# Optimization experiments

Hardware: AMD Instinct MI355X
Metric: run time of the kernel (lower is better)

The kernel has to match this reference:

```python
import jax, jax.numpy as jnp
import numpy as np


def _gru_dirs(x, h, w_ih, w_hh, b_ih, b_hh):
    # One GRU step for both directions at once (seq_len==1 per original loop).
    # x: [N, in], h: [2, N, H]; w_ih: [2, 3H, in], w_hh: [2, 3H, H], biases [2, 3H]
    gi = jnp.einsum('ni,dgi->dng', x, w_ih) + b_ih[:, None, :]
    gh = jnp.einsum('dnh,dgh->dng', h, w_hh) + b_hh[:, None, :]
    H = h.shape[-1]
    ir, iz, inn = gi[..., :H], gi[..., H:2 * H], gi[..., 2 * H:]
    hr, hz, hn = gh[..., :H], gh[..., H:2 * H], gh[..., 2 * H:]
    r = jax.nn.sigmoid(ir + hr)
    z = jax.nn.sigmoid(iz + hz)
    n = jnp.tanh(inn + r * hn)
    return (1.0 - z) * n + z * h


def setup_inputs() -> dict:
    key = jax.random.key(0)
    ks = jax.random.split(key, 6)
    V, E, H, NL = 32000, 1024, 512, 2  # vocab, input_size, hidden_size, num_layers
    N, L = 32, 512
    s = 0.05
    x = jax.random.randint(ks[0], (N, L), 0, V)
    emb = jax.random.normal(ks[1], (V, E), dtype=jnp.float32) * s
    w_ih = jax.random.normal(ks[2], (NL, 2, 3 * H, E), dtype=jnp.float32) * s
    w_hh = jax.random.normal(ks[3], (NL, 2, 3 * H, H), dtype=jnp.float32) * s
    b_ih = jax.random.normal(ks[4], (NL, 2, 3 * H), dtype=jnp.float32) * s
    b_hh = jax.random.normal(ks[5], (NL, 2, 3 * H), dtype=jnp.float32) * s
    return {"x": x, "emb": emb, "w_ih": w_ih, "w_hh": w_hh, "b_ih": b_ih, "b_hh": b_hh}


def reference(x, emb, w_ih, w_hh, b_ih, b_hh):
    # Because the torch code calls the bidirectional GRU one timestep at a time
    # with a carried hidden, BOTH directions scan left-to-right over the sequence.
    N, L = x.shape
    num_layers = w_ih.shape[0]
    H = w_hh.shape[-1]
    h0 = jnp.zeros((num_layers, 2, N, H), dtype=emb.dtype)

    def step(h, xt):
        layer_in = emb[xt]  # [N, E] embedding lookup for this timestep
        new_h = []
        for l in range(num_layers):  # fixed small layer loop
            hl = _gru_dirs(layer_in, h[l], w_ih[l], w_hh[l], b_ih[l], b_hh[l])
            new_h.append(hl)
            layer_in = jnp.concatenate([hl[0], hl[1]], axis=-1)  # [N, 2H]
        hs = jnp.stack(new_h)  # [num_layers, 2, N, H]
        return hs, (layer_in, hs)

    _, (outs, hiddens) = jax.lax.scan(step, h0, x.T)  # scan over L timesteps
    outputs = jnp.transpose(outs, (1, 0, 2))  # [N, L, 2H]
    hiddens = hiddens.reshape(L, num_layers * 2, N, H)  # [L, 2*num_layers, N, H]
    return outputs, hiddens
```

## Files before the change

### kernel.cpp

```cpp
#include <hip/hip_runtime.h>
#include <hip/hip_bf16.h>

using u16 = unsigned short;
using u32 = unsigned int;
using bf16x8 = __attribute__((ext_vector_type(8))) __bf16;
using f32x4  = __attribute__((ext_vector_type(4))) float;
using u32x4  = __attribute__((ext_vector_type(4))) u32;

#define GLP(p) ((const __attribute__((address_space(1))) void*)(p))
#define LDSP(p) ((__attribute__((address_space(3))) void*)(p))

__device__ __forceinline__ float bf2f(u16 u) {
    union { float f; u32 i; } v; v.i = ((u32)u) << 16; return v.f;
}
__device__ __forceinline__ u16 f2bf(float f) {
    union { float f; u32 i; } v; v.f = f;
    u32 r = v.i + 0x7FFFu + ((v.i >> 16) & 1u);
    return (u16)(r >> 16);
}

__device__ __forceinline__ u32 ld_sc01_u32(const u32* p) {
    u32 v;
    asm volatile("global_load_dword %0, %1, off sc0 sc1\n\ts_waitcnt vmcnt(0)"
                 : "=v"(v) : "v"(p) : "memory");
    return v;
}
__device__ __forceinline__ void st_sc01_u32(u32* p, u32 v) {
    asm volatile("global_store_dword %0, %1, off sc0 sc1" :: "v"(p), "v"(v) : "memory");
}
__device__ __forceinline__ void st_sc01_u16(u16* p, u16 v) {
    asm volatile("global_store_short %0, %1, off sc0 sc1" :: "v"(p), "v"(v) : "memory");
}
__device__ __forceinline__ void st_sc01_u32x4(u16* p, u32x4 v) {
    asm volatile("global_store_dwordx4 %0, %1, off sc0 sc1" :: "v"(p), "v"(v) : "memory");
}

__global__ void k_gather(const int* __restrict__ x, const float* __restrict__ emb,
                         u16* __restrict__ X0) {
    int gid = blockIdx.x * blockDim.x + threadIdx.x;
    if (gid >= 16384 * 256) return;
    int e4 = gid << 2;
    int m = e4 >> 10, k = e4 & 1023;
    int t = m >> 5, n = m & 31;
    int tok = x[n * 512 + t];
    float4 v = *reinterpret_cast<const float4*>(emb + ((size_t)tok << 10) + k);
    ushort4 o;
    o.x = f2bf(v.x); o.y = f2bf(v.y); o.z = f2bf(v.z); o.w = f2bf(v.w);
    *reinterpret_cast<ushort4*>(X0 + (size_t)e4) = o;
}

__global__ void k_f32bf16(const float* __restrict__ s, u16* __restrict__ d, int n4) {
    int gid = blockIdx.x * blockDim.x + threadIdx.x;
    if (gid >= n4) return;
    float4 v = reinterpret_cast<const float4*>(s)[gid];
    ushort4 o;
    o.x = f2bf(v.x); o.y = f2bf(v.y); o.z = f2bf(v.z); o.w = f2bf(v.w);
    reinterpret_cast<ushort4*>(d)[gid] = o;
}

template<int LAYER>
__device__ __forceinline__ void gru_body(char* smem, int d, int wg,
    const u16* __restrict__ Gi, const u16* __restrict__ Whh_l,
    const float* __restrict__ bhh_l, u16* __restrict__ hbuf,
    u16* __restrict__ X1, float* __restrict__ hid, float* __restrict__ outp,
    u32* __restrict__ flags, u32* __restrict__ xflags, const u32* __restrict__ gdone)
{
    char* hS          = smem;
    float (*ghs)[196] = (float(*)[196])(smem + 32768);
    u16 (*gis)[208]   = (u16(*)[208])(smem + 57856);
    float* bhh_s      = (float*)(smem + 71168);
    u16* hvS          = (u16*)(smem + 71936);
    const int tid = threadIdx.x;
    const int lane = tid & 63, w = tid >> 6;
    const int j0 = wg * 64;
    const int g = w >> 2;
    const int lr = lane & 15, lk = lane >> 4;

    if (tid < 192) {
        int g2 = tid >> 6, jj = tid & 63;
        bhh_s[tid] = bhh_l[d * 1536 + g2 * 512 + j0 + jj];
    }
    bf16x8 wf[16];
    {
        const int joff = (w & 3) * 16;
        const u16* wr = Whh_l + (size_t)(d * 1536 + g * 512 + j0 + joff + lr) * 512 + lk * 8;
        #pragma unroll
        for (int kt = 0; kt < 16; ++kt)
            wf[kt] = *reinterpret_cast<const bf16x8*>(wr + kt * 32);
    }
    __syncthreads();

    u32* myflag = flags + (d * 8 + wg) * 32;
    const u32* wflag = flags + (d * 8 + (w & 7)) * 32;
    u32* myxflag = (LAYER == 0) ? xflags + (d * 8 + wg) * 32 : nullptr;

    const int c8 = (lane & 7) * 8;
    const int rb = lane >> 3;
    const int colu = w * 64 + c8;
    const int ci0 = (tid - 512) * 3;

    float hp0 = 0.f, hp1 = 0.f, hp2 = 0.f;
    u32 g_seen = 0;

    for (int t = 0; t < 512; ++t) {
        if (w < 8) {
            if (t > 0) {
                long long tt0 = __builtin_amdgcn_s_memrealtime();
                while (ld_sc01_u32(wflag) < (u32)t) {
                    __builtin_amdgcn_s_sleep(1);
                    if (__builtin_amdgcn_s_memrealtime() - tt0 > 2000) {
                        if (lane == 0)
                            __hip_atomic_store(myflag, (u32)t, __ATOMIC_RELEASE,
                                               __HIP_MEMORY_SCOPE_AGENT);
                        tt0 = __builtin_amdgcn_s_memrealtime();
                    }
                }
            }
            const u16* hb = hbuf + ((size_t)d * 2 + ((t + 1) & 1)) * 16384;
            u32x4 v0, v1, v2, v3;
            asm volatile("global_load_dwordx4 %0, %1, off sc0 sc1"
                         : "=v"(v0) : "v"(hb + (size_t)(rb)      * 512 + colu));
            asm volatile("global_load_dwordx4 %0, %1, off sc0 sc1"
                         : "=v"(v1) : "v"(hb + (size_t)(rb + 8)  * 512 + colu));
            asm volatile("global_load_dwordx4 %0, %1, off sc0 sc1"
                         : "=v"(v2) : "v"(hb + (size_t)(rb + 16) * 512 + colu));
            asm volatile("global_load_dwordx4 %0, %1, off sc0 sc1"
                         : "=v"(v3) : "v"(hb + (size_t)(rb + 24) * 512 + colu));
            asm volatile("s_waitcnt vmcnt(0)" ::: "memory");
            const int cb = colu * 2;
            *reinterpret_cast<u32x4*>(hS + (rb)      * 1024 + (cb ^ (((rb)      & 15) << 4))) = v0;
            *reinterpret_cast<u32x4*>(hS + (rb + 8)  * 1024 + (cb ^ (((rb + 8)  & 15) << 4))) = v1;
            *reinterpret_cast<u32x4*>(hS + (rb + 16) * 1024 + (cb ^ (((rb + 16) & 15) << 4))) = v2;
            *reinterpret_cast<u32x4*>(hS + (rb + 24) * 1024 + (cb ^ (((rb + 24) & 15) << 4))) = v3;
        } else {
            u32 yneed = (u32)(t >> 2);
            if (g_seen <= yneed) {
                const u32* gp = gdone + yneed;
                long long T0 = __builtin_amdgcn_s_memrealtime();
                while (ld_sc01_u32(gp) == 0) {
                    __builtin_amdgcn_s_sleep(1);
                    if (__builtin_amdgcn_s_memrealtime() - T0 > 2000000) break;
                }
                g_seen = yneed + 1;
            }
            u32x4 gq[3];
            int nbs[3], gcs[3];
            #pragma unroll
            for (int i = 0; i < 3; ++i) {
                int ci = ci0 + i;
                nbs[i] = ci / 24; gcs[i] = ci % 24;
                const u16* gp = Gi + (size_t)(t * 32 + nbs[i]) * 3072 + d * 1536
                              + (gcs[i] >> 3) * 512 + j0 + (gcs[i] & 7) * 8;
                asm volatile("global_load_dwordx4 %0, %1, off sc0 sc1"
                             : "=v"(gq[i]) : "v"(gp));
            }
            asm volatile("s_waitcnt vmcnt(0)" ::: "memory");
            #pragma unroll
            for (int i = 0; i < 3; ++i)
                *reinterpret_cast<u32x4*>(&gis[nbs[i]][gcs[i] * 8]) = gq[i];
        }
        __syncthreads();

        f32x4 acc0 = {0.f, 0.f, 0.f, 0.f}, acc1 = acc0;
        #pragma unroll
        for (int kt = 0; kt < 16; ++kt) {
            int boff = (lk * 16 + kt * 64) ^ (lr << 4);
            bf16x8 a0 = *reinterpret_cast<const bf16x8*>(hS + lr * 1024 + boff);
            bf16x8 a1 = *reinterpret_cast<const bf16x8*>(hS + (16 + lr) * 1024 + boff);
            acc0 = __builtin_amdgcn_mfma_f32_16x16x32_bf16(a0, wf[kt], acc0, 0, 0, 0);
            acc1 = __builtin_amdgcn_mfma_f32_16x16x32_bf16(a1, wf[kt], acc1, 0, 0, 0);
        }
        int colg = w * 16 + lr;
        float bv = bhh_s[colg];
        #pragma unroll
        for (int q = 0; q < 4; ++q) {
            ghs[lk * 4 + q][colg]      = acc0[q] + bv;
            ghs[16 + lk * 4 + q][colg] = acc1[q] + bv;
        }
        __syncthreads();

        u16* hbw = hbuf + ((size_t)d * 2 + (t & 1)) * 16384;
        #pragma unroll
        for (int rep = 0; rep < 3; ++rep) {
            int e = tid + rep * 768;
            if (e < 2048) {
                int j = e & 63, nb = e >> 6;
                float gr = bf2f(gis[nb][j])       + ghs[nb][j];
                float gz = bf2f(gis[nb][64 + j])  + ghs[nb][64 + j];
                float r = 1.f / (1.f + __expf(-gr));
                float z = 1.f / (1.f + __expf(-gz));
                float ng = tanhf(bf2f(gis[nb][128 + j]) + r * ghs[nb][128 + j]);
                float hp = (rep == 0) ? hp0 : (rep == 1) ? hp1 : hp2;
                float hv = (1.f - z) * ng + z * hp;
                if (rep == 0) hp0 = hv; else if (rep == 1) hp1 = hv; else hp2 = hv;
                u16 hb16 = f2bf(hv);
                st_sc01_u16(hbw + (size_t)nb * 512 + j0 + j, hb16);
                hvS[nb * 64 + j] = hb16;
            }
        }
        asm volatile("s_waitcnt vmcnt(0)" ::: "memory");
        __syncthreads();
        if (tid == 16)
            st_sc01_u32(myflag, (u32)(t + 1));

        if (tid >= 512) {
            int q = tid - 512, nb = q >> 3, j8 = (q & 7) * 8;
            union { u32x4 v; u16 s[8]; } h8;
            h8.v = *reinterpret_cast<const u32x4*>(hvS + nb * 64 + j8);
            float f0 = bf2f(h8.s[0]), f1 = bf2f(h8.s[1]), f2 = bf2f(h8.s[2]), f3 = bf2f(h8.s[3]);
            float f4 = bf2f(h8.s[4]), f5 = bf2f(h8.s[5]), f6 = bf2f(h8.s[6]), f7 = bf2f(h8.s[7]);
            float* hp = hid + ((size_t)(t * 4 + LAYER * 2 + d) * 32 + nb) * 512 + j0 + j8;
            *reinterpret_cast<float4*>(hp)     = make_float4(f0, f1, f2, f3);
            *reinterpret_cast<float4*>(hp + 4) = make_float4(f4, f5, f6, f7);
            if (LAYER == 0) {
                u16* xp = X1 + (size_t)(t * 32 + nb) * 1024 + (size_t)d * 512 + j0 + j8;
                st_sc01_u32x4(xp, h8.v);
            } else {
                float* op = outp + ((size_t)nb * 512 + t) * 1024 + (size_t)d * 512 + j0 + j8;
                *reinterpret_cast<float4*>(op)     = make_float4(f0, f1, f2, f3);
                *reinterpret_cast<float4*>(op + 4) = make_float4(f4, f5, f6, f7);
            }
        }
        if (LAYER == 0 && (t & 3) == 3) {
            asm volatile("s_waitcnt vmcnt(0)" ::: "memory");
            __syncthreads();
            if (tid == 17)
                st_sc01_u32(myxflag, (u32)(t + 1));
        }
    }
}

__device__ __forceinline__ void chaser_body(char* smem, int cw,
    const u16* __restrict__ A, const u16* __restrict__ B,
    const float* __restrict__ bias, u16* __restrict__ Gi,
    const u32* __restrict__ xflags, u32* __restrict__ cnt, u32* __restrict__ done)
{
    u16* As = (u16*)smem;
    u16* Bs = (u16*)(smem + 16384);
    const int tid = threadIdx.x;
    const int lane = tid & 63, wid = tid >> 6;
    const int wm = wid & 1, wn = wid >> 1;
    const int lr = lane & 15, lk = lane >> 4;

    for (int T = cw; T < 4096; T += 48) {
        const int y = T >> 5, x = T & 31;
        if (xflags && tid < 16) {
            const u32* fp = xflags + tid * 32;
            u32 target = 4u * (u32)y + 4u;
            long long T0 = __builtin_amdgcn_s_memrealtime();
            while (ld_sc01_u32(fp) < target) {
                __builtin_amdgcn_s_sleep(4);
                if (__builtin_amdgcn_s_memrealtime() - T0 > 2000000) break;
            }
        }
        __syncthreads();

        f32x4 zero = {0.f, 0.f, 0.f, 0.f};
        f32x4 acc[4][2];
        #pragma unroll
        for (int i = 0; i < 4; ++i) { acc[i][0] = zero; acc[i][1] = zero; }

        for (int k0 = 0; k0 < 1024; k0 += 64) {
            #pragma unroll
            for (int r = 0; r < 5; ++r) {
                int c = wid * 5 + r;
                if (c < 16) {
                    int o = c * 1024 + lane * 16;
                    int row = o >> 7, kb = o & 127;
                    int kbs = kb ^ ((row & 7) << 4);
                    const char* s = (const char*)A + ((size_t)(y * 128 + row) * 1024 + k0) * 2 + kbs;
                    __builtin_amdgcn_global_load_lds(GLP(s), LDSP((char*)As + c * 1024), 16, 0, 0);
                } else if (c < 28) {
                    int c2 = c - 16;
                    int o = c2 * 1024 + lane * 16;
                    int row = o >> 7, kb = o & 127;
                    int kbs = kb ^ ((row & 7) << 4);
                    const char* s = (const char*)B + ((size_t)(x * 96 + row) * 1024 + k0) * 2 + kbs;
                    __builtin_amdgcn_global_load_lds(GLP(s), LDSP((char*)Bs + c2 * 1024), 16, 0, 0);
                }
            }
            __syncthreads();
            if (wid < 6) {
                #pragma unroll
                for (int kk = 0; kk < 2; ++kk) {
                    bf16x8 af[4], bfr[2];
                    int kb = kk * 64 + lk * 16;
                    #pragma unroll
                    for (int i = 0; i < 4; ++i) {
                        int rowA = wm * 64 + i * 16 + lr;
                        af[i] = *reinterpret_cast<const bf16x8*>((const char*)As + rowA * 128 + (kb ^ ((rowA & 7) << 4)));
                    }
                    #pragma unroll
                    for (int j = 0; j < 2; ++j) {
                        int rowB = wn * 32 + j * 16 + lr;
                        bfr[j] = *reinterpret_cast<const bf16x8*>((const char*)Bs + rowB * 128 + (kb ^ ((rowB & 7) << 4)));
                    }
                    #pragma unroll
                    for (int i = 0; i < 4; ++i)
                        #pragma unroll
                        for (int j = 0; j < 2; ++j)
                            acc[i][j] = __builtin_amdgcn_mfma_f32_16x16x32_bf16(af[i], bfr[j], acc[i][j], 0, 0, 0);
                }
            }
            __syncthreads();
        }
        if (wid < 6) {
            #pragma unroll
            for (int j = 0; j < 2; ++j) {
                int col = x * 96 + wn * 32 + j * 16 + lr;
                float bv = bias[col];
                #pragma unroll
                for (int i = 0; i < 4; ++i) {
                    int rowb = y * 128 + wm * 64 + i * 16 + lk * 4;
                    #pragma unroll
                    for (int q = 0; q < 4; ++q)
                        st_sc01_u16(Gi + (size_t)(rowb + q) * 3072 + col, f2bf(acc[i][j][q] + bv));
                }
            }
        }
        asm volatile("s_waitcnt vmcnt(0)" ::: "memory");
        __syncthreads();
        if (tid == 0) {
            u32 old = __hip_atomic_fetch_add(&cnt[y], 1u, __ATOMIC_RELAXED,
                                             __HIP_MEMORY_SCOPE_AGENT);
            if (old == 31u)
                st_sc01_u32((u32*)&done[y], 1u);
        }
    }
}

__global__ __launch_bounds__(768, 2) void k_fused(
    u16* __restrict__ Gi,
    const u16* __restrict__ X0, const u16* __restrict__ Wih,
    const float* __restrict__ b_ih,
    const u16* __restrict__ Whh, const float* __restrict__ bhh,
    u16* __restrict__ hbuf0, u16* __restrict__ hbuf1,
    u16* __restrict__ X1,
    float* __restrict__ hid, float* __restrict__ outp,
    u32* __restrict__ flags0, u32* __restrict__ flags1,
    u32* __restrict__ xflags,
    u32* __restrict__ g0cnt, u32* __restrict__ g0done,
    u32* __restrict__ g1cnt, u32* __restrict__ g1done)
{
    __shared__ __align__(16) char smem[76032];
    int bid = blockIdx.x;
    if (bid < 16) {
        gru_body<0>(smem, bid >> 3, bid & 7, Gi, Whh, bhh, hbuf0,
                    X1, hid, outp, flags0, xflags, g0done);
    } else if (bid < 64) {
        chaser_body(smem, bid - 16, X0, Wih, b_ih, Gi, nullptr, g0cnt, g0done);
    } else if (bid < 112) {
        chaser_body(smem, bid - 64, X1, Wih + (size_t)3072 * 1024, b_ih + 3072,
                    Gi, xflags, g1cnt, g1done);
    } else {
        int b = bid - 112;
        gru_body<1>(smem, b >> 3, b & 7, Gi, Whh + (size_t)3072 * 512, bhh + 3072,
                    hbuf1, nullptr, hid, outp, flags1, nullptr, g1done);
    }
}

extern "C" void kernel_launch(void* const* d_in, const int* in_sizes, int n_in,
                              void* d_out, int out_size, void* d_ws, size_t ws_size,
                              hipStream_t stream) {
    const int*   x    = (const int*)d_in[0];
    const float* emb  = (const float*)d_in[1];
    const float* w_ih = (const float*)d_in[2];
    const float* w_hh = (const float*)d_in[3];
    const float* b_ih = (const float*)d_in[4];
    const float* b_hh = (const float*)d_in[5];
    float* outp = (float*)d_out;
    float* hid  = outp + (size_t)32 * 512 * 1024;

    char* ws = (char*)d_ws;
    u16* X0     = (u16*)(ws);
    u16* X1     = (u16*)(ws + 33554432);
    u16* Wih    = (u16*)(ws + 67108864);
    u16* Whh    = (u16*)(ws + 79691776);
    u16* Gi     = (u16*)(ws + 85983232);
    u16* hbuf0  = (u16*)(ws + 186646528);
    u16* hbuf1  = (u16*)(ws + 186777600);
    u32* flags0 = (u32*)(ws + 186908672);
    u32* flags1 = (u32*)(ws + 186910720);
    u32* xflags = (u32*)(ws + 186912768);
    u32* g0cnt  = (u32*)(ws + 186914816);
    u32* g0done = (u32*)(ws + 186915328);
    u32* g1cnt  = (u32*)(ws + 186915840);
    u32* g1done = (u32*)(ws + 186916352);

    k_gather<<<16384, 256, 0, stream>>>(x, emb, X0);
    k_f32bf16<<<(1572864 + 255) / 256, 256, 0, stream>>>(w_ih, Wih, 1572864);
    k_f32bf16<<<( 786432 + 255) / 256, 256, 0, stream>>>(w_hh, Whh, 786432);

    (void)hipMemsetAsync(hbuf0, 0, 270336, stream);

    k_fused<<<128, 768, 0, stream>>>(Gi, X0, Wih, b_ih, Whh, b_hh,
                                     hbuf0, hbuf1, X1, hid, outp,
                                     flags0, flags1, xflags,
                                     g0cnt, g0done, g1cnt, g1done);
}
```

Before: 2.141 ms.

## Replace per-step block barrier with per-wave LDS ready flags and fast gates

Each wave that loads a slice of h into LDS now posts its own ready flag. The MFMA loop spins on each flag before consuming that k-slice, so the full __syncthreads before the recurrent matmul is gone and compute can start while other slices are still arriving. The global flag spin drops s_sleep and checks the timer only every 16 polls. The gate math switches to rcp/exp-based sigmoid and tanh and handles two outputs per thread, storing them as packed u32. This targets latency on the serial recurrence, at the cost of busier LDS and global spinning and slightly less accurate activations.

```diff
diff --git a/kernel.cpp b/kernel.cpp
--- a/kernel.cpp
+++ b/kernel.cpp
@@ -33,6 +33,14 @@
 }
 __device__ __forceinline__ void st_sc01_u32x4(u16* p, u32x4 v) {
     asm volatile("global_store_dwordx4 %0, %1, off sc0 sc1" :: "v"(p), "v"(v) : "memory");
+}
+
+__device__ __forceinline__ float sigm(float x) {
+    return __builtin_amdgcn_rcpf(1.f + __expf(-x));
+}
+__device__ __forceinline__ float tanh_fast(float x) {
+    float e = __expf(-2.f * x);
+    return (1.f - e) * __builtin_amdgcn_rcpf(1.f + e);
 }
 
 __global__ void k_gather(const int* __restrict__ x, const float* __restrict__ emb,
@@ -70,6 +78,7 @@
     u16 (*gis)[208]   = (u16(*)[208])(smem + 57856);
     float* bhh_s      = (float*)(smem + 71168);
     u16* hvS          = (u16*)(smem + 71936);
+    volatile u32* rdy = (volatile u32*)(smem + 76032);
     const int tid = threadIdx.x;
     const int lane = tid & 63, w = tid >> 6;
     const int j0 = wg * 64;
@@ -80,6 +89,7 @@
         int g2 = tid >> 6, jj = tid & 63;
         bhh_s[tid] = bhh_l[d * 1536 + g2 * 512 + j0 + jj];
     }
+    if (tid < 8) rdy[tid] = 0;
     bf16x8 wf[16];
     {
         const int joff = (w & 3) * 16;
@@ -92,27 +102,29 @@
 
     u32* myflag = flags + (d * 8 + wg) * 32;
     const u32* wflag = flags + (d * 8 + (w & 7)) * 32;
-    u32* myxflag = (LAYER == 0) ? xflags + (d * 8 + wg) * 32 : nullptr;
 
     const int c8 = (lane & 7) * 8;
     const int rb = lane >> 3;
     const int colu = w * 64 + c8;
     const int ci0 = (tid - 512) * 3;
 
-    float hp0 = 0.f, hp1 = 0.f, hp2 = 0.f;
+    float hpv[4] = {0.f, 0.f, 0.f, 0.f};
     u32 g_seen = 0;
 
     for (int t = 0; t < 512; ++t) {
         if (w < 8) {
             if (t > 0) {
                 long long tt0 = __builtin_amdgcn_s_memrealtime();
+                int k = 0;
                 while (ld_sc01_u32(wflag) < (u32)t) {
-                    __builtin_amdgcn_s_sleep(1);
-                    if (__builtin_amdgcn_s_memrealtime() - tt0 > 2000) {
-                        if (lane == 0)
-                            __hip_atomic_store(myflag, (u32)t, __ATOMIC_RELEASE,
-                                               __HIP_MEMORY_SCOPE_AGENT);
-                        tt0 = __builtin_amdgcn_s_memrealtime();
+                    if (++k >= 16) {
+                        k = 0;
+                        if (__builtin_amdgcn_s_memrealtime() - tt0 > 2000) {
+                            if (lane == 0)
+                                __hip_atomic_store(myflag, (u32)t, __ATOMIC_RELEASE,
+                                                   __HIP_MEMORY_SCOPE_AGENT);
+                            tt0 = __builtin_amdgcn_s_memrealtime();
+                        }
                     }
                 }
             }
@@ -132,6 +144,9 @@
             *reinterpret_cast<u32x4*>(hS + (rb + 8)  * 1024 + (cb ^ (((rb + 8)  & 15) << 4))) = v1;
             *reinterpret_cast<u32x4*>(hS + (rb + 16) * 1024 + (cb ^ (((rb + 16) & 15) << 4))) = v2;
             *reinterpret_cast<u32x4*>(hS + (rb + 24) * 1024 + (cb ^ (((rb + 24) & 15) << 4))) = v3;
+            asm volatile("s_waitcnt lgkmcnt(0)" ::: "memory");
+            __builtin_amdgcn_sched_barrier(0);
+            if (lane == 0) rdy[w] = (u32)(t + 1);
         } else {
             u32 yneed = (u32)(t >> 2);
             if (g_seen <= yneed) {
@@ -159,16 +174,22 @@
             for (int i = 0; i < 3; ++i)
                 *reinterpret_cast<u32x4*>(&gis[nbs[i]][gcs[i] * 8]) = gq[i];
         }
-        __syncthreads();
 
         f32x4 acc0 = {0.f, 0.f, 0.f, 0.f}, acc1 = acc0;
         #pragma unroll
-        for (int kt = 0; kt < 16; ++kt) {
-            int boff = (lk * 16 + kt * 64) ^ (lr << 4);
-            bf16x8 a0 = *reinterpret_cast<const bf16x8*>(hS + lr * 1024 + boff);
-            bf16x8 a1 = *reinterpret_cast<const bf16x8*>(hS + (16 + lr) * 1024 + boff);
-            acc0 = __builtin_amdgcn_mfma_f32_16x16x32_bf16(a0, wf[kt], acc0, 0, 0, 0);
-            acc1 = __builtin_amdgcn_mfma_f32_16x16x32_bf16(a1, wf[kt], acc1, 0, 0, 0);
+        for (int s = 0; s < 8; ++s) {
+            while (rdy[s] < (u32)(t + 1)) {}
+            __builtin_amdgcn_sched_barrier(0);
+            int b0 = (lk * 16 + (2 * s) * 64) ^ (lr << 4);
+            int b1 = (lk * 16 + (2 * s + 1) * 64) ^ (lr << 4);
+            bf16x8 a00 = *reinterpret_cast<const bf16x8*>(hS + lr * 1024 + b0);
+            bf16x8 a10 = *reinterpret_cast<const bf16x8*>(hS + (16 + lr) * 1024 + b0);
+            bf16x8 a01 = *reinterpret_cast<const bf16x8*>(hS + lr * 1024 + b1);
+            bf16x8 a11 = *reinterpret_cast<const bf16x8*>(hS + (16 + lr) * 1024 + b1);
+            acc0 = __builtin_amdgcn_mfma_f32_16x16x32_bf16(a00, wf[2 * s],     acc0, 0, 0, 0);
+            acc1 = __builtin_amdgcn_mfma_f32_16x16x32_bf16(a10, wf[2 * s],     acc1, 0, 0, 0);
+            acc0 = __builtin_amdgcn_mfma_f32_16x16x32_bf16(a01, wf[2 * s + 1], acc0, 0, 0, 0);
+            acc1 = __builtin_amdgcn_mfma_f32_16x16x32_bf16(a11, wf[2 * s + 1], acc1, 0, 0, 0);
         }
         int colg = w * 16 + lr;
         float bv = bhh_s[colg];
@@ -181,21 +202,22 @@
 
         u16* hbw = hbuf + ((size_t)d * 2 + (t & 1)) * 16384;
         #pragma unroll
-        for (int rep = 0; rep < 3; ++rep) {
-            int e = tid + rep * 768;
-            if (e < 2048) {
-                int j = e & 63, nb = e >> 6;
-                float gr = bf2f(gis[nb][j])       + ghs[nb][j];
-                float gz = bf2f(gis[nb][64 + j])  + ghs[nb][64 + j];
-                float r = 1.f / (1.f + __expf(-gr));
-                float z = 1.f / (1.f + __expf(-gz));
-                float ng = tanhf(bf2f(gis[nb][128 + j]) + r * ghs[nb][128 + j]);
-                float hp = (rep == 0) ? hp0 : (rep == 1) ? hp1 : hp2;
-                float hv = (1.f - z) * ng + z * hp;
-                if (rep == 0) hp0 = hv; else if (rep == 1) hp1 = hv; else hp2 = hv;
-                u16 hb16 = f2bf(hv);
-                st_sc01_u16(hbw + (size_t)nb * 512 + j0 + j, hb16);
-                hvS[nb * 64 + j] = hb16;
+        for (int rep = 0; rep < 2; ++rep) {
+            int e2 = tid + rep * 768;
+            if (e2 < 1024) {
+                int jp = (e2 & 31) * 2, nb = e2 >> 5;
+                float r0 = sigm(bf2f(gis[nb][jp])      + ghs[nb][jp]);
+                float r1 = sigm(bf2f(gis[nb][jp + 1])  + ghs[nb][jp + 1]);
+                float z0 = sigm(bf2f(gis[nb][64 + jp])     + ghs[nb][64 + jp]);
+                float z1 = sigm(bf2f(gis[nb][64 + jp + 1]) + ghs[nb][64 + jp + 1]);
+                float n0 = tanh_fast(bf2f(gis[nb][128 + jp])     + r0 * ghs[nb][128 + jp]);
+                float n1 = tanh_fast(bf2f(gis[nb][128 + jp + 1]) + r1 * ghs[nb][128 + jp + 1]);
+                float hv0 = (1.f - z0) * n0 + z0 * hpv[rep * 2];
+                float hv1 = (1.f - z1) * n1 + z1 * hpv[rep * 2 + 1];
+                hpv[rep * 2] = hv0; hpv[rep * 2 + 1] = hv1;
+                u32 packed = (u32)f2bf(hv0) | ((u32)f2bf(hv1) << 16);
+                st_sc01_u32((u32*)(hbw + (size_t)nb * 512 + j0 + jp), packed);
+                *reinterpret_cast<u32*>(hvS + nb * 64 + jp) = packed;
             }
         }
         asm volatile("s_waitcnt vmcnt(0)" ::: "memory");
@@ -225,7 +247,7 @@
             asm volatile("s_waitcnt vmcnt(0)" ::: "memory");
             __syncthreads();
             if (tid == 17)
-                st_sc01_u32(myxflag, (u32)(t + 1));
+                st_sc01_u32(xflags + (d * 8 + wg) * 32, (u32)(t + 1));
         }
     }
 }
@@ -342,7 +364,7 @@
     u32* __restrict__ g0cnt, u32* __restrict__ g0done,
     u32* __restrict__ g1cnt, u32* __restrict__ g1done)
 {
-    __shared__ __align__(16) char smem[76032];
+    __shared__ __align__(16) char smem[76096];
     int bid = blockIdx.x;
     if (bid < 16) {
         gru_body<0>(smem, bid >> 3, bid & 7, Gi, Whh, bhh, hbuf0,
```

Result: slower. 2.322 ms (+8.5%).
